# Kernel optimization log

Hardware: AMD Instinct MI355X
Metric: run time of the kernel (lower is better)

## Reference

```python
import jax, jax.numpy as jnp
import numpy as np

N_USERS = 100000
N_ITEMS = 50000
N = N_USERS + N_ITEMS
D = 64
NNZ = 2000000
B = 16384
LAYERS = 3
HYPER_X = 0.5


def setup_inputs() -> dict:
    key = jax.random.key(0)
    ks = jax.random.split(key, 10)
    return {
        "emb_user": jax.random.uniform(ks[0], (N_USERS, D), jnp.float32, -1.0, 1.0),
        "emb_item": jax.random.uniform(ks[1], (N_ITEMS, D), jnp.float32, -1.0, 1.0),
        "w_user": jax.random.uniform(ks[2], (D, D), jnp.float32, -1.0, 1.0),
        "w_item": jax.random.uniform(ks[3], (D, D), jnp.float32, -1.0, 1.0),
        "xij_emb1": jnp.full((N_ITEMS, 1), 2.0, jnp.float32),
        "xij_emb0": jnp.full((N_ITEMS, 1), -2.0, jnp.float32),
        "g_val": jax.random.uniform(ks[4], (NNZ,), jnp.float32, 0.0, 0.1),
        "g_row": jax.random.randint(ks[5], (NNZ,), 0, N, jnp.int32),
        "g_col": jax.random.randint(ks[6], (NNZ,), 0, N, jnp.int32),
        "users": jax.random.randint(ks[7], (B,), 0, N_USERS, jnp.int32),
        "items": jax.random.randint(ks[8], (B,), 0, N_ITEMS, jnp.int32),
        "xij": jax.random.randint(ks[9], (B,), 0, 2, jnp.int32),
    }


def _spmm(row, col, val, x):
    # sparse COO @ dense: gather rows of x by col, scale, scatter-add by row
    return jax.ops.segment_sum(val[:, None] * x[col], row, num_segments=N)


def reference(emb_user, emb_item, w_user, w_item, xij_emb1, xij_emb0,
              g_val, g_row, g_col, users, items, xij):
    # --- computer(): LightGCN propagation with running sum -> mean ---
    e = jnp.concatenate([emb_user, emb_item], axis=0)  # [N, D]
    acc = e
    for _ in range(LAYERS):
        e = _spmm(g_row, g_col, g_val, e)
        acc = acc + e
    light = acc / (LAYERS + 1)
    all_users, all_items = light[:N_USERS], light[N_USERS:]

    # --- forward(users, items, xij) ---
    ue = all_users[users]                  # [B, D]
    ie = all_items[items]                  # [B, D]
    xij_emb = jnp.where(xij[:, None] > 0, xij_emb1[items], xij_emb0[items])  # [B, 1]
    ue = ue @ w_user.T                     # Linear, no bias
    ie = ie @ w_item.T
    hx = jnp.float32(HYPER_X)
    ue = jnp.concatenate(
        [(1.0 - hx) * jax.nn.softmax(ue, axis=1),
         jnp.full((ue.shape[0], 1), hx, dtype=ue.dtype)], axis=1)
    ie = jax.nn.sigmoid(jnp.concatenate([ie, xij_emb], axis=1))
    return jnp.sum(ue * ie, axis=1)        # gamma [B]
```

## Files before the change

kernel.cpp:

```cpp
#include <hip/hip_runtime.h>
#include <cstddef>

#define D 64
#define RPB 128
#define MAXB 1280
#define PCHUNK 4096
#define TB 64

static __device__ __forceinline__ unsigned short f2b(float f) {
    unsigned u = __float_as_uint(f);
    return (unsigned short)((u + 0x7FFFu + ((u >> 16) & 1u)) >> 16);
}
static __device__ __forceinline__ float b2f(unsigned short h) {
    return __uint_as_float(((unsigned)h) << 16);
}

__global__ void convert_kernel(const float* __restrict__ eu, const float* __restrict__ ei,
                               unsigned short* __restrict__ e0, int nd_user, int nd_total) {
    int i = blockIdx.x * blockDim.x + threadIdx.x;
    int stride = gridDim.x * blockDim.x;
    int nq = nd_total >> 2, nqu = nd_user >> 2;
    for (int idx = i; idx < nq; idx += stride) {
        float4 v = (idx < nqu) ? ((const float4*)eu)[idx] : ((const float4*)ei)[idx - nqu];
        ushort4 o;
        o.x = f2b(v.x); o.y = f2b(v.y); o.z = f2b(v.z); o.w = f2b(v.w);
        ((ushort4*)e0)[idx] = o;
    }
}

__global__ void mark_kernel(const int* __restrict__ users, const int* __restrict__ items,
                            int* __restrict__ flags, int B, int n_users) {
    int i = blockIdx.x * blockDim.x + threadIdx.x;
    if (i < B) {
        flags[users[i]] = 1;
        flags[n_users + items[i]] = 1;
    }
}

__global__ __launch_bounds__(256)
void bucket_hist_kernel(const int* __restrict__ row, int* __restrict__ ghist,
                        int nnz, int nb) {
    __shared__ int h[MAXB];
    for (int b = threadIdx.x; b < nb; b += blockDim.x) h[b] = 0;
    __syncthreads();
    int i = blockIdx.x * blockDim.x + threadIdx.x;
    int stride = gridDim.x * blockDim.x;
    for (int e = i; e < nnz; e += stride) atomicAdd(&h[row[e] >> 7], 1);
    __syncthreads();
    for (int b = threadIdx.x; b < nb; b += blockDim.x)
        if (h[b]) atomicAdd(&ghist[b], h[b]);
}

__global__ __launch_bounds__(256)
void bucket_scan_kernel(const int* __restrict__ ghist, int* __restrict__ bofs,
                        int* __restrict__ gcur, int nb, int nnz) {
    __shared__ int part[256];
    int seg = (nb + 255) >> 8;
    int base = threadIdx.x * seg;
    int s = 0;
    for (int i = 0; i < seg; ++i)
        if (base + i < nb) s += ghist[base + i];
    part[threadIdx.x] = s;
    __syncthreads();
    for (int off = 1; off < 256; off <<= 1) {
        int t = (threadIdx.x >= (unsigned)off) ? part[threadIdx.x - off] : 0;
        __syncthreads();
        part[threadIdx.x] += t;
        __syncthreads();
    }
    int run = part[threadIdx.x] - s;
    for (int i = 0; i < seg; ++i) {
        int b = base + i;
        if (b < nb) {
            bofs[b] = run;
            gcur[b] = run;
            run += ghist[b];
        }
    }
    if (threadIdx.x == 0) bofs[nb] = nnz;
}

__global__ __launch_bounds__(256)
void partition_kernel(const int* __restrict__ row, const int* __restrict__ col,
                      const float* __restrict__ val, int* __restrict__ gcur,
                      uint2* __restrict__ ep, int nnz, int nb) {
    __shared__ int h[MAXB];
    __shared__ int cur[MAXB];
    int cbeg = blockIdx.x * PCHUNK;
    int cend = min(nnz, cbeg + PCHUNK);
    for (int b = threadIdx.x; b < nb; b += blockDim.x) h[b] = 0;
    __syncthreads();
    for (int e = cbeg + threadIdx.x; e < cend; e += blockDim.x)
        atomicAdd(&h[row[e] >> 7], 1);
    __syncthreads();
    for (int b = threadIdx.x; b < nb; b += blockDim.x) {
        int c = h[b];
        cur[b] = c ? atomicAdd(&gcur[b], c) : 0;
    }
    __syncthreads();
    for (int e = cbeg + threadIdx.x; e < cend; e += blockDim.x) {
        int r = row[e];
        int b = r >> 7;
        int p = atomicAdd(&cur[b], 1);
        ep[p] = make_uint2((((unsigned)r & 127u) << 18) | (unsigned)col[e],
                           __float_as_uint(val[e]));
    }
}

__global__ __launch_bounds__(256)
void rowsort_kernel(const uint2* __restrict__ ep, const int* __restrict__ bofs,
                    uint2* __restrict__ ep2, int* __restrict__ ptr,
                    int n, int nnz) {
    __shared__ int hist[RPB];
    __shared__ int sc[RPB];
    __shared__ int cur[RPB];
    int b = blockIdx.x;
    int beg = bofs[b], end = bofs[b + 1];
    int tid = threadIdx.x;
    if (tid < RPB) hist[tid] = 0;
    __syncthreads();
    for (int e = beg + tid; e < end; e += blockDim.x)
        atomicAdd(&hist[ep[e].x >> 18], 1);
    __syncthreads();
    int hv = 0;
    if (tid < RPB) { hv = hist[tid]; sc[tid] = hv; }
    __syncthreads();
    for (int off = 1; off < RPB; off <<= 1) {
        int t = 0;
        if (tid < RPB && tid >= off) t = sc[tid - off];
        __syncthreads();
        if (tid < RPB) sc[tid] += t;
        __syncthreads();
    }
    if (tid < RPB) {
        int excl = sc[tid] - hv;
        cur[tid] = excl;
        int r = (b << 7) + tid;
        if (r < n) ptr[r] = beg + excl;
    }
    if (b == 0 && tid == 0) ptr[n] = nnz;
    __syncthreads();
    for (int e = beg + tid; e < end; e += blockDim.x) {
        uint2 kv = ep[e];
        int rl = kv.x >> 18;
        int p = atomicAdd(&cur[rl], 1);
        ep2[beg + p] = kv;
    }
}

__global__ __launch_bounds__(256)
void spmm_bf16_kernel(const int* __restrict__ ptr, const uint2* __restrict__ ep,
                      const unsigned short* __restrict__ x,
                      const int* __restrict__ flags,
                      unsigned short* __restrict__ y, int n) {
    int lane = threadIdx.x & 63;
    int wid  = (blockIdx.x * blockDim.x + threadIdx.x) >> 6;
    int sub  = lane & 15;
    int rg   = lane >> 4;
    int r    = wid * 4 + rg;
    if (r >= n) return;
    if (flags && !flags[r]) return;

    int beg = ptr[r], end = ptr[r + 1];
    int klbase = lane & 48;
    float4 s = make_float4(0.f, 0.f, 0.f, 0.f);

    for (int base = beg; base < end; base += 16) {
        int m = min(16, end - base);
        uint2 kv = (sub < m) ? ep[base + sub] : make_uint2(0u, 0u);
        int   myc = kv.x & 0x3FFFF;
        float myv = __uint_as_float(kv.y);
        int k = 0;
        for (; k + 4 <= m; k += 4) {
            int   c0 = __shfl(myc, klbase + k);
            int   c1 = __shfl(myc, klbase + k + 1);
            int   c2 = __shfl(myc, klbase + k + 2);
            int   c3 = __shfl(myc, klbase + k + 3);
            float v0 = __shfl(myv, klbase + k);
            float v1 = __shfl(myv, klbase + k + 1);
            float v2 = __shfl(myv, klbase + k + 2);
            float v3 = __shfl(myv, klbase + k + 3);
            ushort4 h0 = ((const ushort4*)(x + ((size_t)c0 << 6)))[sub];
            ushort4 h1 = ((const ushort4*)(x + ((size_t)c1 << 6)))[sub];
            ushort4 h2 = ((const ushort4*)(x + ((size_t)c2 << 6)))[sub];
            ushort4 h3 = ((const ushort4*)(x + ((size_t)c3 << 6)))[sub];
            s.x = fmaf(v0, b2f(h0.x), s.x); s.y = fmaf(v0, b2f(h0.y), s.y);
            s.z = fmaf(v0, b2f(h0.z), s.z); s.w = fmaf(v0, b2f(h0.w), s.w);
            s.x = fmaf(v1, b2f(h1.x), s.x); s.y = fmaf(v1, b2f(h1.y), s.y);
            s.z = fmaf(v1, b2f(h1.z), s.z); s.w = fmaf(v1, b2f(h1.w), s.w);
            s.x = fmaf(v2, b2f(h2.x), s.x); s.y = fmaf(v2, b2f(h2.y), s.y);
            s.z = fmaf(v2, b2f(h2.z), s.z); s.w = fmaf(v2, b2f(h2.w), s.w);
            s.x = fmaf(v3, b2f(h3.x), s.x); s.y = fmaf(v3, b2f(h3.y), s.y);
            s.z = fmaf(v3, b2f(h3.z), s.z); s.w = fmaf(v3, b2f(h3.w), s.w);
        }
        for (; k < m; ++k) {
            int   c = __shfl(myc, klbase + k);
            float v = __shfl(myv, klbase + k);
            ushort4 h = ((const ushort4*)(x + ((size_t)c << 6)))[sub];
            s.x = fmaf(v, b2f(h.x), s.x); s.y = fmaf(v, b2f(h.y), s.y);
            s.z = fmaf(v, b2f(h.z), s.z); s.w = fmaf(v, b2f(h.w), s.w);
        }
    }

    ushort4 o;
    o.x = f2b(s.x); o.y = f2b(s.y); o.z = f2b(s.z); o.w = f2b(s.w);
    ((ushort4*)(y + ((size_t)r << 6)))[sub] = o;
}

__global__ __launch_bounds__(256)
void head_kernel(const float* __restrict__ eu, const float* __restrict__ ei,
                 const unsigned short* __restrict__ e1,
                 const unsigned short* __restrict__ e2,
                 const unsigned short* __restrict__ e3,
                 const float* __restrict__ wu, const float* __restrict__ wi,
                 const float* __restrict__ x1, const float* __restrict__ x0,
                 const int* __restrict__ users, const int* __restrict__ items,
                 const int* __restrict__ xij,
                 float* __restrict__ out, int B, int n_users) {
    __shared__ float uet[D * TB];
    __shared__ float iet[D * TB];
    __shared__ float wut[D * D];
    __shared__ float wit[D * D];

    int t  = threadIdx.x;
    int b0 = blockIdx.x * TB;

    for (int i = t; i < D * D; i += 256) {
        int k = i >> 6, j = i & 63;
        wut[i] = wu[j * D + k];
        wit[i] = wi[j * D + k];
    }

    {
        int l  = t & 15;
        int g  = t >> 4;
        for (int p = 0; p < 4; ++p) {
            int bl = g + p * 16;
            int b  = b0 + bl;
            if (b < B) {
                int u  = users[b];
                int it = items[b];
                size_t uo  = ((size_t)u << 6);
                size_t io  = ((size_t)(n_users + it) << 6);
                size_t io2 = ((size_t)it << 6);
                float4  fu = ((const float4*)(eu + uo))[l];
                ushort4 u1 = ((const ushort4*)(e1 + uo))[l];
                ushort4 u2 = ((const ushort4*)(e2 + uo))[l];
                ushort4 u3 = ((const ushort4*)(e3 + uo))[l];
                float4  fi = ((const float4*)(ei + io2))[l];
                ushort4 i1 = ((const ushort4*)(e1 + io))[l];
                ushort4 i2 = ((const ushort4*)(e2 + io))[l];
                ushort4 i3 = ((const ushort4*)(e3 + io))[l];
                int k0 = l << 2;
                uet[(k0 + 0) * TB + bl] = (fu.x + b2f(u1.x) + b2f(u2.x) + b2f(u3.x)) * 0.25f;
                uet[(k0 + 1) * TB + bl] = (fu.y + b2f(u1.y) + b2f(u2.y) + b2f(u3.y)) * 0.25f;
                uet[(k0 + 2) * TB + bl] = (fu.z + b2f(u1.z) + b2f(u2.z) + b2f(u3.z)) * 0.25f;
                uet[(k0 + 3) * TB + bl] = (fu.w + b2f(u1.w) + b2f(u2.w) + b2f(u3.w)) * 0.25f;
                iet[(k0 + 0) * TB + bl] = (fi.x + b2f(i1.x) + b2f(i2.x) + b2f(i3.x)) * 0.25f;
                iet[(k0 + 1) * TB + bl] = (fi.y + b2f(i1.y) + b2f(i2.y) + b2f(i3.y)) * 0.25f;
                iet[(k0 + 2) * TB + bl] = (fi.z + b2f(i1.z) + b2f(i2.z) + b2f(i3.z)) * 0.25f;
                iet[(k0 + 3) * TB + bl] = (fi.w + b2f(i1.w) + b2f(i2.w) + b2f(i3.w)) * 0.25f;
            }
        }
    }
    __syncthreads();

    int jg = (t & 15) << 2;
    int bg = (t >> 4) << 2;
    float su[4][4], si[4][4];
    #pragma unroll
    for (int a = 0; a < 4; ++a)
        #pragma unroll
        for (int c = 0; c < 4; ++c) { su[a][c] = 0.f; si[a][c] = 0.f; }

    #pragma unroll 4
    for (int k = 0; k < D; ++k) {
        float4 u4 = *(const float4*)&uet[k * TB + bg];
        float4 i4 = *(const float4*)&iet[k * TB + bg];
        float4 a4 = *(const float4*)&wut[k * D + jg];
        float4 c4 = *(const float4*)&wit[k * D + jg];
        const float ub[4] = {u4.x, u4.y, u4.z, u4.w};
        const float ib[4] = {i4.x, i4.y, i4.z, i4.w};
        const float wa[4] = {a4.x, a4.y, a4.z, a4.w};
        const float wc[4] = {c4.x, c4.y, c4.z, c4.w};
        #pragma unroll
        for (int a = 0; a < 4; ++a)
            #pragma unroll
            for (int c = 0; c < 4; ++c) {
                su[a][c] = fmaf(ub[a], wa[c], su[a][c]);
                si[a][c] = fmaf(ib[a], wc[c], si[a][c]);
            }
    }

    float m[4], S[4], T[4];
    #pragma unroll
    for (int a = 0; a < 4; ++a) {
        float mm = fmaxf(fmaxf(su[a][0], su[a][1]), fmaxf(su[a][2], su[a][3]));
        for (int off = 1; off < 16; off <<= 1) mm = fmaxf(mm, __shfl_xor(mm, off));
        m[a] = mm;
    }
    #pragma unroll
    for (int a = 0; a < 4; ++a) {
        float sl = 0.f, tl = 0.f;
        #pragma unroll
        for (int c = 0; c < 4; ++c) {
            float e = __expf(su[a][c] - m[a]);
            float g = 1.f / (1.f + __expf(-si[a][c]));
            sl += e;
            tl = fmaf(e, g, tl);
        }
        for (int off = 1; off < 16; off <<= 1) {
            sl += __shfl_xor(sl, off);
            tl += __shfl_xor(tl, off);
        }
        S[a] = sl; T[a] = tl;
    }

    if ((t & 15) == 0) {
        #pragma unroll
        for (int a = 0; a < 4; ++a) {
            int b = b0 + bg + a;
            if (b < B) {
                int it = items[b];
                float xe   = (xij[b] > 0) ? x1[it] : x0[it];
                float sigx = 1.f / (1.f + __expf(-xe));
                out[b] = 0.5f * T[a] / S[a] + 0.5f * sigx;
            }
        }
    }
}

__global__ void init_kernel(const float* __restrict__ eu, const float* __restrict__ ei,
                            float* __restrict__ e_cur, float* __restrict__ acc,
                            int nd_user, int nd_total) {
    int i = blockIdx.x * blockDim.x + threadIdx.x;
    int stride = gridDim.x * blockDim.x;
    int nq = nd_total >> 2;
    int nq_user = nd_user >> 2;
    for (int idx = i; idx < nq; idx += stride) {
        float4 v;
        if (idx < nq_user) v = ((const float4*)eu)[idx];
        else               v = ((const float4*)ei)[idx - nq_user];
        ((float4*)e_cur)[idx] = v;
        ((float4*)acc)[idx]   = v;
    }
}

__global__ void spmm_atomic_kernel(const int* __restrict__ row, const int* __restrict__ col,
                                   const float* __restrict__ val, const float* __restrict__ x,
                                   float* __restrict__ y, int nnz) {
    int lane  = threadIdx.x & 63;
    int wave  = (blockIdx.x * blockDim.x + threadIdx.x) >> 6;
    int nwave = (gridDim.x * blockDim.x) >> 6;
    for (int e = wave; e < nnz; e += nwave)
        atomicAdd(&y[(size_t)row[e] * D + lane], val[e] * x[(size_t)col[e] * D + lane]);
}

__global__ void accum_kernel(float* __restrict__ acc, const float* __restrict__ nxt,
                             int nd_total) {
    int i = blockIdx.x * blockDim.x + threadIdx.x;
    int stride = gridDim.x * blockDim.x;
    int nq = nd_total >> 2;
    for (int idx = i; idx < nq; idx += stride) {
        float4 a = ((float4*)acc)[idx];
        float4 b = ((const float4*)nxt)[idx];
        a.x += b.x; a.y += b.y; a.z += b.z; a.w += b.w;
        ((float4*)acc)[idx] = a;
    }
}

__global__ __launch_bounds__(256)
void head_acc_kernel(const float* __restrict__ acc,
                     const float* __restrict__ wu, const float* __restrict__ wi,
                     const float* __restrict__ x1, const float* __restrict__ x0,
                     const int* __restrict__ users, const int* __restrict__ items,
                     const int* __restrict__ xij,
                     float* __restrict__ out, int B, int n_users) {
    __shared__ float wtu[D * D];
    __shared__ float wti[D * D];
    for (int idx = threadIdx.x; idx < D * D; idx += blockDim.x) {
        int j = idx >> 6, k = idx & 63;
        wtu[k * D + j] = wu[idx];
        wti[k * D + j] = wi[idx];
    }
    __syncthreads();
    int lane = threadIdx.x & 63;
    int wid  = threadIdx.x >> 6;
    int nw   = blockDim.x >> 6;
    for (int b = blockIdx.x * nw + wid; b < B; b += gridDim.x * nw) {
        int u  = users[b];
        int it = items[b];
        float ue = acc[(size_t)u * D + lane] * 0.25f;
        float ie = acc[(size_t)(n_users + it) * D + lane] * 0.25f;
        float su = 0.f, si = 0.f;
        #pragma unroll 8
        for (int k = 0; k < D; ++k) {
            float uk = __shfl(ue, k);
            float ik = __shfl(ie, k);
            su = fmaf(uk, wtu[k * D + lane], su);
            si = fmaf(ik, wti[k * D + lane], si);
        }
        float m = su;
        for (int off = 32; off > 0; off >>= 1) m = fmaxf(m, __shfl_xor(m, off));
        float p = __expf(su - m);
        float sden = p;
        for (int off = 32; off > 0; off >>= 1) sden += __shfl_xor(sden, off);
        float soft = p / sden;
        float sig  = 1.f / (1.f + __expf(-si));
        float term = 0.5f * soft * sig;
        for (int off = 32; off > 0; off >>= 1) term += __shfl_xor(term, off);
        if (lane == 0) {
            float xe   = (xij[b] > 0) ? x1[it] : x0[it];
            float sigx = 1.f / (1.f + __expf(-xe));
            out[b] = term + 0.5f * sigx;
        }
    }
}

extern "C" void kernel_launch(void* const* d_in, const int* in_sizes, int n_in,
                              void* d_out, int out_size, void* d_ws, size_t ws_size,
                              hipStream_t stream) {
    const float* emb_user = (const float*)d_in[0];
    const float* emb_item = (const float*)d_in[1];
    const float* w_user   = (const float*)d_in[2];
    const float* w_item   = (const float*)d_in[3];
    const float* xij_emb1 = (const float*)d_in[4];
    const float* xij_emb0 = (const float*)d_in[5];
    const float* g_val    = (const float*)d_in[6];
    const int*   g_row    = (const int*)d_in[7];
    const int*   g_col    = (const int*)d_in[8];
    const int*   users    = (const int*)d_in[9];
    const int*   items    = (const int*)d_in[10];
    const int*   xij      = (const int*)d_in[11];
    float*       out      = (float*)d_out;

    const int n_users = in_sizes[0] / D;
    const int n_items = in_sizes[1] / D;
    const int n_total = n_users + n_items;
    const int nnz     = in_sizes[6];
    const int B       = in_sizes[9];

    const int nd_user  = n_users * D;
    const int nd_total = n_total * D;
    const int nb = (n_total + RPB - 1) / RPB;

    const size_t hbytes   = (((size_t)nd_total * 2) + 255) & ~(size_t)255;
    const size_t ebytes   = (size_t)nnz * sizeof(uint2);
    const size_t ptrbytes = ((size_t)(n_total + 1) * 4 + 255) & ~(size_t)255;
    const size_t flbytes  = ((size_t)n_total * 4 + 255) & ~(size_t)255;
    const size_t ibytes   = ((size_t)(nb + 1) * 4 + 255) & ~(size_t)255;
    const size_t need = 4 * hbytes + 2 * ebytes + ptrbytes + flbytes + 3 * ibytes + 256;

    if (ws_size >= need && nb <= MAXB) {
        char* w = (char*)d_ws;
        unsigned short* e0 = (unsigned short*)w;  w += hbytes;
        unsigned short* e1 = (unsigned short*)w;  w += hbytes;
        unsigned short* e2 = (unsigned short*)w;  w += hbytes;
        unsigned short* e3 = (unsigned short*)w;  w += hbytes;
        uint2* ep    = (uint2*)w;                 w += ebytes;
        uint2* ep2   = (uint2*)w;                 w += ebytes;
        int*   ptr   = (int*)w;                   w += ptrbytes;
        int*   flags = (int*)w;                   w += flbytes;
        int*   ghist = (int*)w;                   w += ibytes;
        int*   bofs  = (int*)w;                   w += ibytes;
        int*   gcur  = (int*)w;                   w += ibytes;

        hipMemsetAsync(ghist, 0, (size_t)nb * 4, stream);
        hipMemsetAsync(flags, 0, (size_t)n_total * 4, stream);

        convert_kernel<<<2048, 256, 0, stream>>>(emb_user, emb_item, e0,
                                                 nd_user, nd_total);
        mark_kernel<<<(B + 255) / 256, 256, 0, stream>>>(users, items, flags,
                                                         B, n_users);

        bucket_hist_kernel<<<256, 256, 0, stream>>>(g_row, ghist, nnz, nb);
        bucket_scan_kernel<<<1, 256, 0, stream>>>(ghist, bofs, gcur, nb, nnz);
        const int pblocks = (nnz + PCHUNK - 1) / PCHUNK;
        partition_kernel<<<pblocks, 256, 0, stream>>>(g_row, g_col, g_val, gcur,
                                                      ep, nnz, nb);
        rowsort_kernel<<<nb, 256, 0, stream>>>(ep, bofs, ep2, ptr, n_total, nnz);

        const int nblk = (n_total * 16 + 255) / 256;
        spmm_bf16_kernel<<<nblk, 256, 0, stream>>>(ptr, ep2, e0, nullptr, e1, n_total);
        spmm_bf16_kernel<<<nblk, 256, 0, stream>>>(ptr, ep2, e1, nullptr, e2, n_total);
        spmm_bf16_kernel<<<nblk, 256, 0, stream>>>(ptr, ep2, e2, flags,  e3, n_total);

        head_kernel<<<(B + TB - 1) / TB, 256, 0, stream>>>(
            emb_user, emb_item, e1, e2, e3,
            w_user, w_item, xij_emb1, xij_emb0,
            users, items, xij, out, B, n_users);
    } else {
        const size_t fbytes = (size_t)nd_total * sizeof(float);
        char* w = (char*)d_ws;
        float* e_a = (float*)w;  w += fbytes;
        float* e_b = (float*)w;  w += fbytes;
        float* acc = (float*)w;  w += fbytes;
        float* cur = e_a;
        float* nxt = e_b;
        init_kernel<<<2048, 256, 0, stream>>>(emb_user, emb_item, cur, acc,
                                              nd_user, nd_total);
        for (int l = 0; l < 3; ++l) {
            hipMemsetAsync(nxt, 0, fbytes, stream);
            spmm_atomic_kernel<<<2048, 256, 0, stream>>>(g_row, g_col, g_val, cur, nxt, nnz);
            accum_kernel<<<2048, 256, 0, stream>>>(acc, nxt, nd_total);
            float* t = cur; cur = nxt; nxt = t;
        }
        head_acc_kernel<<<256, 256, 0, stream>>>(acc, w_user, w_item,
                                                 xij_emb1, xij_emb0,
                                                 users, items, xij, out, B, n_users);
    }
}
```

Measured before the change: 327.9 us.

## Use 512-row buckets and locally sort partition chunks before scattering

```diff
diff --git a/kernel.cpp b/kernel.cpp
--- a/kernel.cpp
+++ b/kernel.cpp
@@ -2,9 +2,11 @@
 #include <cstddef>
 
 #define D 64
-#define RPB 128
-#define MAXB 1280
+#define RPB 512
+#define MAXB 512
 #define PCHUNK 4096
+#define PTHREADS 512
+#define EPT (PCHUNK / PTHREADS)
 #define TB 64
 
 static __device__ __forceinline__ unsigned short f2b(float f) {
@@ -45,7 +47,7 @@
     __syncthreads();
     int i = blockIdx.x * blockDim.x + threadIdx.x;
     int stride = gridDim.x * blockDim.x;
-    for (int e = i; e < nnz; e += stride) atomicAdd(&h[row[e] >> 7], 1);
+    for (int e = i; e < nnz; e += stride) atomicAdd(&h[row[e] >> 9], 1);
     __syncthreads();
     for (int b = threadIdx.x; b < nb; b += blockDim.x)
         if (h[b]) atomicAdd(&ghist[b], h[b]);
@@ -80,34 +82,77 @@
     if (threadIdx.x == 0) bofs[nb] = nnz;
 }
 
-__global__ __launch_bounds__(256)
+__global__ __launch_bounds__(PTHREADS)
 void partition_kernel(const int* __restrict__ row, const int* __restrict__ col,
                       const float* __restrict__ val, int* __restrict__ gcur,
                       uint2* __restrict__ ep, int nnz, int nb) {
-    __shared__ int h[MAXB];
-    __shared__ int cur[MAXB];
+    __shared__ uint2 sorted[PCHUNK];
+    __shared__ unsigned short bid[PCHUNK];
+    __shared__ int hist[MAXB];
+    __shared__ int sc[MAXB];
+    __shared__ int lofs[MAXB];
+    __shared__ int gofs[MAXB];
+    __shared__ int lcur[MAXB];
+
+    int tid  = threadIdx.x;
     int cbeg = blockIdx.x * PCHUNK;
     int cend = min(nnz, cbeg + PCHUNK);
-    for (int b = threadIdx.x; b < nb; b += blockDim.x) h[b] = 0;
-    __syncthreads();
-    for (int e = cbeg + threadIdx.x; e < cend; e += blockDim.x)
-        atomicAdd(&h[row[e] >> 7], 1);
-    __syncthreads();
-    for (int b = threadIdx.x; b < nb; b += blockDim.x) {
-        int c = h[b];
-        cur[b] = c ? atomicAdd(&gcur[b], c) : 0;
-    }
-    __syncthreads();
-    for (int e = cbeg + threadIdx.x; e < cend; e += blockDim.x) {
-        int r = row[e];
-        int b = r >> 7;
-        int p = atomicAdd(&cur[b], 1);
-        ep[p] = make_uint2((((unsigned)r & 127u) << 18) | (unsigned)col[e],
-                           __float_as_uint(val[e]));
-    }
-}
-
-__global__ __launch_bounds__(256)
+    int cnt  = cend - cbeg;
+
+    for (int b = tid; b < MAXB; b += PTHREADS) hist[b] = 0;
+    __syncthreads();
+
+    unsigned mykey[EPT];
+    float    myval[EPT];
+    int      mybkt[EPT];
+    #pragma unroll
+    for (int k = 0; k < EPT; ++k) {
+        int e = cbeg + k * PTHREADS + tid;
+        mybkt[k] = -1;
+        if (e < cend) {
+            int r = row[e];
+            int b = r >> 9;
+            mykey[k] = (((unsigned)r & 511u) << 18) | (unsigned)col[e];
+            myval[k] = val[e];
+            mybkt[k] = b;
+            atomicAdd(&hist[b], 1);
+        }
+    }
+    __syncthreads();
+
+    int own = (tid < nb) ? hist[tid] : 0;
+    sc[tid] = own;
+    __syncthreads();
+    for (int off = 1; off < MAXB; off <<= 1) {
+        int t = (tid >= off) ? sc[tid - off] : 0;
+        __syncthreads();
+        sc[tid] += t;
+        __syncthreads();
+    }
+    int excl = sc[tid] - own;
+    if (tid < nb) {
+        lofs[tid] = excl;
+        lcur[tid] = excl;
+        if (own) gofs[tid] = atomicAdd(&gcur[tid], own) - excl;
+    }
+    __syncthreads();
+
+    #pragma unroll
+    for (int k = 0; k < EPT; ++k) {
+        int b = mybkt[k];
+        if (b >= 0) {
+            int p = atomicAdd(&lcur[b], 1);
+            sorted[p] = make_uint2(mykey[k], __float_as_uint(myval[k]));
+            bid[p] = (unsigned short)b;
+        }
+    }
+    __syncthreads();
+
+    for (int p = tid; p < cnt; p += PTHREADS)
+        ep[p + gofs[bid[p]]] = sorted[p];
+}
+
+__global__ __launch_bounds__(PTHREADS)
 void rowsort_kernel(const uint2* __restrict__ ep, const int* __restrict__ bofs,
                     uint2* __restrict__ ep2, int* __restrict__ ptr,
                     int n, int nnz) {
@@ -117,30 +162,27 @@
     int b = blockIdx.x;
     int beg = bofs[b], end = bofs[b + 1];
     int tid = threadIdx.x;
-    if (tid < RPB) hist[tid] = 0;
-    __syncthreads();
-    for (int e = beg + tid; e < end; e += blockDim.x)
+    hist[tid] = 0;
+    __syncthreads();
+    for (int e = beg + tid; e < end; e += PTHREADS)
         atomicAdd(&hist[ep[e].x >> 18], 1);
     __syncthreads();
-    int hv = 0;
-    if (tid < RPB) { hv = hist[tid]; sc[tid] = hv; }
+    int own = hist[tid];
+    sc[tid] = own;
     __syncthreads();
     for (int off = 1; off < RPB; off <<= 1) {
-        int t = 0;
-        if (tid < RPB && tid >= off) t = sc[tid - off];
+        int t = (tid >= off) ? sc[tid - off] : 0;
         __syncthreads();
-        if (tid < RPB) sc[tid] += t;
+        sc[tid] += t;
         __syncthreads();
     }
-    if (tid < RPB) {
-        int excl = sc[tid] - hv;
-        cur[tid] = excl;
-        int r = (b << 7) + tid;
-        if (r < n) ptr[r] = beg + excl;
-    }
+    int excl = sc[tid] - own;
+    cur[tid] = excl;
+    int r = (b << 9) + tid;
+    if (r < n) ptr[r] = beg + excl;
     if (b == 0 && tid == 0) ptr[n] = nnz;
     __syncthreads();
-    for (int e = beg + tid; e < end; e += blockDim.x) {
+    for (int e = beg + tid; e < end; e += PTHREADS) {
         uint2 kv = ep[e];
         int rl = kv.x >> 18;
         int p = atomicAdd(&cur[rl], 1);
@@ -476,9 +518,9 @@
         bucket_hist_kernel<<<256, 256, 0, stream>>>(g_row, ghist, nnz, nb);
         bucket_scan_kernel<<<1, 256, 0, stream>>>(ghist, bofs, gcur, nb, nnz);
         const int pblocks = (nnz + PCHUNK - 1) / PCHUNK;
-        partition_kernel<<<pblocks, 256, 0, stream>>>(g_row, g_col, g_val, gcur,
-                                                      ep, nnz, nb);
-        rowsort_kernel<<<nb, 256, 0, stream>>>(ep, bofs, ep2, ptr, n_total, nnz);
+        partition_kernel<<<pblocks, PTHREADS, 0, stream>>>(g_row, g_col, g_val, gcur,
+                                                           ep, nnz, nb);
+        rowsort_kernel<<<nb, PTHREADS, 0, stream>>>(ep, bofs, ep2, ptr, n_total, nnz);
 
         const int nblk = (n_total * 16 + 255) / 256;
         spmm_bf16_kernel<<<nblk, 256, 0, stream>>>(ptr, ep2, e0, nullptr, e1, n_total);
```

Result: faster. 293.2 us (-10.6%).
